# Optimization experiments

Measured on AMD Instinct MI355X. Metric: run time of the kernel, lower is better.

## Reference

```python
import jax, jax.numpy as jnp
from jax import lax
import numpy as np

B, H, W, C = 64, 64, 64, 8          # batch, grid, channel_n (C=8 is structurally required)
PC = 3 * C                           # perceive output channels = 24
FIRE_RATE = 0.5
ALPHA_THR = 0.1

def _conv(x, w, b, padding):
    y = lax.conv_general_dilated(x, w, (1, 1), padding,
                                 dimension_numbers=('NHWC', 'HWIO', 'NHWC'))
    return y + b

def _dwconv(x, k):
    # k: [kh, kw, Cin, mult] (TF depthwise layout) -> grouped conv rhs [kh, kw, 1, Cin*mult]
    kh, kw, cin, m = k.shape
    rhs = k.reshape(kh, kw, 1, cin * m)
    return lax.conv_general_dilated(x, rhs, (1, 1), 'SAME',
                                    dimension_numbers=('NHWC', 'HWIO', 'NHWC'),
                                    feature_group_count=cin)

def _maxpool3(a):
    return lax.reduce_window(a, -jnp.inf, lax.max, (1, 3, 3, 1), (1, 1, 1, 1), 'SAME')

def setup_inputs() -> dict:
    key = jax.random.key(0)
    ks = jax.random.split(key, 12)
    d_flat = H * W * PC                       # 98304
    d_att = 3 * 3 * 24 * 3                    # 648
    s = lambda *sh: 0.02
    return {
        'x': jax.random.normal(ks[0], (B, H, W, C), jnp.float32),
        'update_noise': jax.random.uniform(ks[1], (B, H, W, 1), jnp.float32),
        'W_att': jax.random.normal(ks[2], (d_flat, d_att), jnp.float32) * 0.002,
        'b_att': jax.random.normal(ks[3], (d_att,), jnp.float32) * 0.02,
        'W1': jax.random.normal(ks[4], (3, 3, 3 * PC, 48), jnp.float32) * 0.05,
        'b1': jax.random.normal(ks[5], (48,), jnp.float32) * 0.02,
        'Wt': jax.random.normal(ks[6], (3, 3, 48, 48), jnp.float32) * 0.05,
        'bt': jax.random.normal(ks[7], (48,), jnp.float32) * 0.02,
        'W2': jax.random.normal(ks[8], (1, 1, 48, 128), jnp.float32) * 0.05,
        'b2': jax.random.normal(ks[9], (128,), jnp.float32) * 0.02,
        'W3': jax.random.normal(ks[10], (1, 1, 128, C), jnp.float32) * 0.05,
        'b3': jax.random.normal(ks[11], (C,), jnp.float32) * 0.02,
    }

def reference(x, update_noise, W_att, b_att, W1, b1, Wt, bt, W2, b2, W3, b3):
    # --- fixed perceive stencil (angle = 0) ---
    ident = np.outer(np.float32([0, 1, 0]), np.float32([0, 1, 0]))
    dxk = np.outer(np.float32([1, 0, 1]), np.float32([1, 0, 1])) / 8.0
    dyk = dxk.T
    k = jnp.stack([jnp.asarray(ident), jnp.asarray(dxk), jnp.asarray(dyk)], -1)  # [3,3,3]
    k = jnp.tile(k[:, :, None, :], (1, 1, C, 1))                                 # [3,3,C,3]

    pre_life = _maxpool3(x[:, :, :, 3:4]) > ALPHA_THR

    y = _dwconv(x, k)                                     # [B,H,W,24]
    # global attention: flatten -> dense -> reshape, take sample 0's kernel
    y_sum = (y.reshape(y.shape[0], -1) @ W_att + b_att).reshape(-1, 3, 3, 24, 3)[0]
    y = _dwconv(y, y_sum)                                 # [B,H,W,72]
    y = y * lax.rsqrt(jnp.maximum(jnp.sum(y * y), 1e-12))  # global l2_normalize

    # dmodel: conv3 VALID -> convT3 VALID -> 1x1 relu -> 1x1
    h = _conv(y, W1, b1, 'VALID')                         # [B,62,62,48]
    h = lax.conv_transpose(h, Wt, (1, 1), 'VALID',
                           dimension_numbers=('NHWC', 'HWIO', 'NHWC')) + bt  # [B,64,64,48]
    h = jax.nn.relu(_conv(h, W2, b2, 'SAME'))             # [B,64,64,128]
    dx_out = _conv(h, W3, b3, 'SAME')                     # [B,64,64,C], step_size = 1.0

    update_mask = (update_noise <= FIRE_RATE).astype(x.dtype)
    x2 = x + dx_out * update_mask

    post_life = _maxpool3(x2[:, :, :, 3:4]) > ALPHA_THR
    life = jnp.logical_and(pre_life, post_life).astype(x.dtype)
    return x2 * life
```

## Files before the change

### kernel.cpp

```cpp
#include <hip/hip_runtime.h>

#define NB 64
#define HW 4096

__global__ __launch_bounds__(256) void k_prep(
    const float* __restrict__ W2, float* __restrict__ W2T) {
  for (int i = threadIdx.x; i < 6144; i += 256) {
    int o = i / 48;
    int c = i - o * 48;
    W2T[i] = W2[c * 128 + o];
  }
}

__global__ __launch_bounds__(256) void k_perceive(
    const float* __restrict__ x, float* __restrict__ y_chw,
    float* __restrict__ y0_hwc, float* __restrict__ prelife,
    float* __restrict__ att_zero) {
  int t = threadIdx.x;
  if (blockIdx.x == 0) {
    for (int i = t; i < 649; i += 256) att_zero[i] = 0.f;
  }
  int pix = blockIdx.x * 256 + t;
  int b = pix >> 12;
  int hw = pix & 4095;
  int h = hw >> 6, w = hw & 63;
  const float* xp = x + (size_t)pix * 8;
  bool hm = h > 0, hp = h < 63, wm = w > 0, wp = w < 63;

  float mx = -1e30f;
  #pragma unroll
  for (int di = -1; di <= 1; ++di) {
    if ((unsigned)(h + di) > 63u) continue;
    #pragma unroll
    for (int dj = -1; dj <= 1; ++dj) {
      if ((unsigned)(w + dj) > 63u) continue;
      mx = fmaxf(mx, xp[(di * 64 + dj) * 8 + 3]);
    }
  }
  prelife[pix] = (mx > 0.1f) ? 1.f : 0.f;

  float* yb = y_chw + (size_t)b * 16 * HW + hw;
  bool b0 = (b == 0);
  #pragma unroll
  for (int c = 0; c < 8; ++c) {
    float ctr = xp[c];
    float a00 = (hm && wm) ? xp[(-65) * 8 + c] : 0.f;
    float a02 = (hm && wp) ? xp[(-63) * 8 + c] : 0.f;
    float a20 = (hp && wm) ? xp[(63) * 8 + c] : 0.f;
    float a22 = (hp && wp) ? xp[(65) * 8 + c] : 0.f;
    float d = (a00 + a02 + a20 + a22) * 0.125f;
    yb[(size_t)(c * 2 + 0) * HW] = ctr;
    yb[(size_t)(c * 2 + 1) * HW] = d;
    if (b0) {
      float* y0p = y0_hwc + hw * 24 + c * 3;
      y0p[0] = ctr; y0p[1] = d; y0p[2] = d;
    }
  }
}

__global__ __launch_bounds__(256) void k_att(
    const float* __restrict__ y0, const float* __restrict__ Watt,
    float* __restrict__ att_acc) {
  int t = threadIdx.x;
  int r0 = blockIdx.x * 128;
  float a0 = 0.f, a1 = 0.f, a2 = 0.f;
  for (int r = 0; r < 128; ++r) {
    float yv = y0[r0 + r];
    const float* wr = Watt + (size_t)(r0 + r) * 648;
    a0 = fmaf(yv, wr[t], a0);
    a1 = fmaf(yv, wr[t + 256], a1);
    if (t < 136) a2 = fmaf(yv, wr[t + 512], a2);
  }
  atomicAdd(att_acc + t, a0);
  atomicAdd(att_acc + t + 256, a1);
  if (t < 136) atomicAdd(att_acc + t + 512, a2);
}

__global__ __launch_bounds__(768) void k_fold(
    const float* __restrict__ W1, const float* __restrict__ att_acc,
    const float* __restrict__ b_att, float* __restrict__ K16) {
  __shared__ float ys[648];
  int t = threadIdx.x;
  for (int i = t; i < 648; i += 768) ys[i] = att_acc[i] + b_att[i];
  __syncthreads();
  int r = blockIdx.x;
  int ri = r / 5, rj = r - ri * 5;
  int p = t / 48;
  int o = t - p * 48;
  int c = p >> 1, tt = p & 1;
  float acc = 0.f;
  for (int ki = 0; ki < 3; ++ki) {
    int qi = ri - ki;
    if ((unsigned)qi > 2u) continue;
    for (int kj = 0; kj < 3; ++kj) {
      int qj = rj - kj;
      if ((unsigned)qj > 2u) continue;
      int k9 = ki * 3 + kj, q9 = qi * 3 + qj;
      const float* wb = W1 + (size_t)(k9 * 72 + 9 * c) * 48 + o;
      const float* yb = ys + q9 * 72 + 9 * c;
      if (tt == 0) {
        #pragma unroll
        for (int m = 0; m < 3; ++m) acc = fmaf(wb[(size_t)m * 48], yb[m], acc);
      } else {
        #pragma unroll
        for (int m = 0; m < 3; ++m) {
          acc = fmaf(wb[(size_t)(3 + m) * 48], yb[3 + m], acc);
          acc = fmaf(wb[(size_t)(6 + m) * 48], yb[6 + m], acc);
        }
      }
    }
  }
  K16[(size_t)(r * 16 + p) * 48 + o] = acc;
}

__global__ __launch_bounds__(256) void k_ssq(
    const float* __restrict__ y_chw, const float* __restrict__ att_acc,
    const float* __restrict__ b_att, float* __restrict__ ssq) {
  __shared__ float ys[648];
  __shared__ float s[16 * 324];
  int t = threadIdx.x;
  for (int i = t; i < 648; i += 256) ys[i] = att_acc[i] + b_att[i];

  int blk = blockIdx.x;
  int b = blk >> 4;
  int tile = blk & 15;
  int i0 = (tile >> 2) * 16;
  int j0 = (tile & 3) * 16;
  const float* yb = y_chw + (size_t)b * 16 * HW;

  for (int idx = t; idx < 16 * 324; idx += 256) {
    int c = idx / 324;
    int pos = idx - c * 324;
    int r = pos / 18, col = pos - r * 18;
    int gr = i0 - 1 + r, gc = j0 - 1 + col;
    bool v = ((unsigned)gr < 64u) && ((unsigned)gc < 64u);
    s[idx] = v ? yb[(size_t)c * HW + gr * 64 + gc] : 0.f;
  }
  __syncthreads();

  int ty = t >> 4, tx = t & 15;
  float local = 0.f;
  for (int c = 0; c < 8; ++c) {
    float tapA[9], tapB[9];
    const float* sa = s + (size_t)(2 * c) * 324 + ty * 18 + tx;
    const float* sb = s + (size_t)(2 * c + 1) * 324 + ty * 18 + tx;
    #pragma unroll
    for (int di = 0; di < 3; ++di)
      #pragma unroll
      for (int dj = 0; dj < 3; ++dj) {
        tapA[di * 3 + dj] = sa[di * 18 + dj];
        tapB[di * 3 + dj] = sb[di * 18 + dj];
      }
    #pragma unroll
    for (int m = 0; m < 3; ++m) {
      float z0 = 0.f, z1 = 0.f, z2 = 0.f;
      #pragma unroll
      for (int k9 = 0; k9 < 9; ++k9) {
        z0 = fmaf(tapA[k9], ys[k9 * 72 + 9 * c + m], z0);
        z1 = fmaf(tapB[k9], ys[k9 * 72 + 9 * c + 3 + m], z1);
        z2 = fmaf(tapB[k9], ys[k9 * 72 + 9 * c + 6 + m], z2);
      }
      local += z0 * z0 + z1 * z1 + z2 * z2;
    }
  }
  #pragma unroll
  for (int off = 32; off; off >>= 1) local += __shfl_down(local, off, 64);
  if ((t & 63) == 0) atomicAdd(ssq, local);
}

__global__ __launch_bounds__(256, 4) void k_conv1f(
    const float* __restrict__ y_chw, const float* __restrict__ K16,
    const float* __restrict__ b1, const float* __restrict__ ssqp,
    float* __restrict__ h1) {
  __shared__ float s[16 * 400];
  int t = threadIdx.x;
  int og = __builtin_amdgcn_readfirstlane(t >> 7);
  int sub = t & 127;
  int ty = sub >> 4, tx = sub & 15;
  int blk = blockIdx.x;
  int b = blk >> 4;
  int tile = blk & 15;
  int i0 = (tile >> 2) * 16; if (i0 > 46) i0 = 46;
  int j0 = (tile & 3) * 16;  if (j0 > 46) j0 = 46;

  const float* yb = y_chw + (size_t)b * 16 * HW;
  for (int idx = t; idx < 16 * 400; idx += 256) {
    int c = idx / 400;
    int pos = idx - c * 400;
    int r = pos / 20, col = pos - r * 20;
    int gr = i0 - 1 + r, gc = j0 - 1 + col;
    bool v = ((unsigned)gr < 64u) && ((unsigned)gc < 64u);
    s[idx] = v ? yb[(size_t)c * HW + gr * 64 + gc] : 0.f;
  }
  __syncthreads();

  float acc0[24], acc1[24];
  #pragma unroll
  for (int o = 0; o < 24; ++o) { acc0[o] = 0.f; acc1[o] = 0.f; }

  for (int c = 0; c < 16; ++c) {
    const float* sc = s + (size_t)c * 400 + ty * 20 + tx;
    #pragma unroll
    for (int ri = 0; ri < 5; ++ri) {
      float t0[5], t1[5];
      #pragma unroll
      for (int rj = 0; rj < 5; ++rj) {
        t0[rj] = sc[ri * 20 + rj];
        t1[rj] = sc[(ri + 8) * 20 + rj];
      }
      #pragma unroll
      for (int rj = 0; rj < 5; ++rj) {
        const float* w = K16 + (size_t)((ri * 5 + rj) * 16 + c) * 48 + og * 24;
        float tv0 = t0[rj], tv1 = t1[rj];
        #pragma unroll
        for (int o = 0; o < 24; ++o) {
          acc0[o] = fmaf(tv0, w[o], acc0[o]);
          acc1[o] = fmaf(tv1, w[o], acc1[o]);
        }
      }
    }
  }
  float inv = rsqrtf(fmaxf(ssqp[0], 1e-12f));
  float* hb = h1 + (size_t)b * 48 * 3844 + (size_t)og * 24 * 3844
            + (i0 + ty) * 62 + (j0 + tx);
  #pragma unroll
  for (int o = 0; o < 24; ++o) {
    float bo = b1[og * 24 + o];
    hb[(size_t)o * 3844] = fmaf(acc0[o], inv, bo);
    hb[(size_t)o * 3844 + 8 * 62] = fmaf(acc1[o], inv, bo);
  }
}

__global__ __launch_bounds__(256, 4) void k_convT(
    const float* __restrict__ h1, const float* __restrict__ Wt,
    const float* __restrict__ bt, float* __restrict__ h2) {
  __shared__ float s[24 * 324];
  int t = threadIdx.x;
  int og = __builtin_amdgcn_readfirstlane(t >> 7);
  int sub = t & 127;
  int ty = sub >> 4, tx = sub & 15;
  int blk = blockIdx.x;
  int b = blk >> 4;
  int tile = blk & 15;
  int i0 = (tile >> 2) * 16;
  int j0 = (tile & 3) * 16;

  float acc0[24], acc1[24];
  #pragma unroll
  for (int o = 0; o < 24; ++o) { acc0[o] = 0.f; acc1[o] = 0.f; }
  const float* hb = h1 + (size_t)b * 48 * 3844;

  for (int c0 = 0; c0 < 48; c0 += 24) {
    __syncthreads();
    for (int idx = t; idx < 24 * 324; idx += 256) {
      int c = idx / 324;
      int pos = idx - c * 324;
      int r = pos / 18, col = pos - r * 18;
      int gr = i0 - 2 + r, gc = j0 - 2 + col;
      bool v = ((unsigned)gr < 62u) && ((unsigned)gc < 62u);
      s[idx] = v ? hb[(size_t)(c0 + c) * 3844 + gr * 62 + gc] : 0.f;
    }
    __syncthreads();
    for (int c = 0; c < 24; ++c) {
      const float* sc = s + c * 324 + ty * 18 + tx;
      float tap0[9], tap1[9];
      #pragma unroll
      for (int di = 0; di < 3; ++di)
        #pragma unroll
        for (int dj = 0; dj < 3; ++dj) {
          tap0[di * 3 + dj] = sc[di * 18 + dj];
          tap1[di * 3 + dj] = sc[(di + 8) * 18 + dj];
        }
      #pragma unroll
      for (int k9 = 0; k9 < 9; ++k9) {
        const float* w = Wt + (size_t)(k9 * 48 + c0 + c) * 48 + og * 24;
        float tv0 = tap0[k9], tv1 = tap1[k9];
        #pragma unroll
        for (int o = 0; o < 24; ++o) {
          acc0[o] = fmaf(tv0, w[o], acc0[o]);
          acc1[o] = fmaf(tv1, w[o], acc1[o]);
        }
      }
    }
  }
  float* ob = h2 + (size_t)b * 48 * HW + (size_t)og * 24 * HW
            + (i0 + ty) * 64 + (j0 + tx);
  #pragma unroll
  for (int o = 0; o < 24; ++o) {
    float bo = bt[og * 24 + o];
    ob[(size_t)o * HW] = acc0[o] + bo;
    ob[(size_t)o * HW + 8 * 64] = acc1[o] + bo;
  }
}

__global__ __launch_bounds__(256) void k_head(
    const float* __restrict__ h2, const float* __restrict__ W2T,
    const float* __restrict__ b2, const float* __restrict__ W3,
    const float* __restrict__ b3, const float* __restrict__ x,
    const float* __restrict__ noise, float* __restrict__ x2,
    float* __restrict__ alpha2) {
  int t = threadIdx.x;
  int pix0 = blockIdx.x * 512 + t;
  int pix1 = pix0 + 256;
  int b = pix0 >> 12;
  int hw0 = pix0 & 4095, hw1 = pix1 & 4095;
  float hr0[48], hr1[48];
  const float* hb = h2 + (size_t)b * 48 * HW;
  #pragma unroll
  for (int c = 0; c < 48; ++c) {
    hr0[c] = hb[(size_t)c * HW + hw0];
    hr1[c] = hb[(size_t)c * HW + hw1];
  }
  float dx0[8], dx1[8];
  #pragma unroll
  for (int k = 0; k < 8; ++k) { dx0[k] = b3[k]; dx1[k] = b3[k]; }
  #pragma unroll 2
  for (int o = 0; o < 128; ++o) {
    float v0 = b2[o], v1 = v0;
    const float* w2 = W2T + o * 48;
    #pragma unroll
    for (int c = 0; c < 48; ++c) {
      v0 = fmaf(hr0[c], w2[c], v0);
      v1 = fmaf(hr1[c], w2[c], v1);
    }
    v0 = fmaxf(v0, 0.f);
    v1 = fmaxf(v1, 0.f);
    const float* w3 = W3 + o * 8;
    #pragma unroll
    for (int k = 0; k < 8; ++k) {
      dx0[k] = fmaf(v0, w3[k], dx0[k]);
      dx1[k] = fmaf(v1, w3[k], dx1[k]);
    }
  }
  float m0 = (noise[pix0] <= 0.5f) ? 1.f : 0.f;
  float m1 = (noise[pix1] <= 0.5f) ? 1.f : 0.f;
  const float* xp0 = x + (size_t)pix0 * 8;
  const float* xp1 = x + (size_t)pix1 * 8;
  float* xo0 = x2 + (size_t)pix0 * 8;
  float* xo1 = x2 + (size_t)pix1 * 8;
  float a30 = 0.f, a31 = 0.f;
  #pragma unroll
  for (int k = 0; k < 8; ++k) {
    float v0 = fmaf(dx0[k], m0, xp0[k]);
    float v1 = fmaf(dx1[k], m1, xp1[k]);
    xo0[k] = v0; xo1[k] = v1;
    if (k == 3) { a30 = v0; a31 = v1; }
  }
  alpha2[pix0] = a30;
  alpha2[pix1] = a31;
}

__global__ __launch_bounds__(256) void k_life(
    const float* __restrict__ x2, const float* __restrict__ alpha2,
    const float* __restrict__ prelife, float* __restrict__ out) {
  int pix = blockIdx.x * 256 + threadIdx.x;
  int hw = pix & 4095;
  int h = hw >> 6, w = hw & 63;
  const float* ab = alpha2 + (size_t)(pix - hw);
  float mx = -1e30f;
  #pragma unroll
  for (int di = -1; di <= 1; ++di) {
    if ((unsigned)(h + di) > 63u) continue;
    #pragma unroll
    for (int dj = -1; dj <= 1; ++dj) {
      if ((unsigned)(w + dj) > 63u) continue;
      mx = fmaxf(mx, ab[(h + di) * 64 + (w + dj)]);
    }
  }
  float life = (mx > 0.1f && prelife[pix] > 0.5f) ? 1.f : 0.f;
  const float* xp = x2 + (size_t)pix * 8;
  float* op = out + (size_t)pix * 8;
  #pragma unroll
  for (int k = 0; k < 8; ++k) op[k] = xp[k] * life;
}

extern "C" void kernel_launch(void* const* d_in, const int* in_sizes, int n_in,
                              void* d_out, int out_size, void* d_ws, size_t ws_size,
                              hipStream_t stream) {
  const float* x     = (const float*)d_in[0];
  const float* noise = (const float*)d_in[1];
  const float* Watt  = (const float*)d_in[2];
  const float* b_att = (const float*)d_in[3];
  const float* W1    = (const float*)d_in[4];
  const float* b1    = (const float*)d_in[5];
  const float* Wt    = (const float*)d_in[6];
  const float* bt    = (const float*)d_in[7];
  const float* W2    = (const float*)d_in[8];
  const float* b2    = (const float*)d_in[9];
  const float* W3    = (const float*)d_in[10];
  const float* b3    = (const float*)d_in[11];
  float* out = (float*)d_out;

  float* ws = (float*)d_ws;
  size_t o_y   = 0;
  size_t o_h1  = o_y + 4194304;
  size_t o_h2  = o_h1 + 11808768;
  size_t o_y0  = o_h2 + 12582912;
  size_t o_pre = o_y0 + 98304;
  size_t o_att = o_pre + 262144;
  size_t o_w2t = o_att + 652;
  size_t o_k16 = o_w2t + 6144;
  float* y_chw   = ws + o_y;
  float* h1_chw  = ws + o_h1;
  float* h2_chw  = ws + o_h2;
  float* y0_hwc  = ws + o_y0;
  float* prelife = ws + o_pre;
  float* att_acc = ws + o_att;
  float* ssq     = ws + o_att + 648;
  float* W2T     = ws + o_w2t;
  float* K16     = ws + o_k16;
  float* x2      = ws + o_y;
  float* alpha2  = ws + o_y + 2097152;

  k_prep<<<1, 256, 0, stream>>>(W2, W2T);
  k_perceive<<<1024, 256, 0, stream>>>(x, y_chw, y0_hwc, prelife, att_acc);
  k_att<<<768, 256, 0, stream>>>(y0_hwc, Watt, att_acc);
  k_fold<<<25, 768, 0, stream>>>(W1, att_acc, b_att, K16);
  k_ssq<<<1024, 256, 0, stream>>>(y_chw, att_acc, b_att, ssq);
  k_conv1f<<<1024, 256, 0, stream>>>(y_chw, K16, b1, ssq, h1_chw);
  k_convT<<<1024, 256, 0, stream>>>(h1_chw, Wt, bt, h2_chw);
  k_head<<<512, 256, 0, stream>>>(h2_chw, W2T, b2, W3, b3, x, noise, x2, alpha2);
  k_life<<<1024, 256, 0, stream>>>(x2, alpha2, prelife, out);
}
```

Measured before the change: 888.4 us.

## Fuse convT with 1x1 head, merge prep and fold into neighbor kernels

The transposed conv output tile is staged in shared memory and consumed directly by the 1x1 relu/1x1 head in the same block. This removes the h2 global write and re-read and one launch. The W2 transpose and the K16 fold move into extra blocks of the perceive and ssq kernels, removing two more launches. The price is a larger shared-memory footprint (48x256 floats) and occupancy lowered to 3 blocks/CU. The head now does one pixel per thread instead of two, so weight loads are reused less.

```diff
diff --git a/kernel.cpp b/kernel.cpp
--- a/kernel.cpp
+++ b/kernel.cpp
@@ -2,21 +2,21 @@
 
 #define NB 64
 #define HW 4096
-
-__global__ __launch_bounds__(256) void k_prep(
-    const float* __restrict__ W2, float* __restrict__ W2T) {
-  for (int i = threadIdx.x; i < 6144; i += 256) {
-    int o = i / 48;
-    int c = i - o * 48;
-    W2T[i] = W2[c * 128 + o];
-  }
-}
 
 __global__ __launch_bounds__(256) void k_perceive(
     const float* __restrict__ x, float* __restrict__ y_chw,
     float* __restrict__ y0_hwc, float* __restrict__ prelife,
-    float* __restrict__ att_zero) {
+    float* __restrict__ att_zero, const float* __restrict__ W2,
+    float* __restrict__ W2T) {
   int t = threadIdx.x;
+  if (blockIdx.x == 1024) {
+    for (int i = t; i < 6144; i += 256) {
+      int o = i / 48;
+      int c = i - o * 48;
+      W2T[i] = W2[c * 128 + o];
+    }
+    return;
+  }
   if (blockIdx.x == 0) {
     for (int i = t; i < 649; i += 256) att_zero[i] = 0.f;
   }
@@ -76,49 +76,52 @@
   if (t < 136) atomicAdd(att_acc + t + 512, a2);
 }
 
-__global__ __launch_bounds__(768) void k_fold(
-    const float* __restrict__ W1, const float* __restrict__ att_acc,
-    const float* __restrict__ b_att, float* __restrict__ K16) {
-  __shared__ float ys[648];
-  int t = threadIdx.x;
-  for (int i = t; i < 648; i += 768) ys[i] = att_acc[i] + b_att[i];
-  __syncthreads();
-  int r = blockIdx.x;
-  int ri = r / 5, rj = r - ri * 5;
-  int p = t / 48;
-  int o = t - p * 48;
-  int c = p >> 1, tt = p & 1;
-  float acc = 0.f;
-  for (int ki = 0; ki < 3; ++ki) {
-    int qi = ri - ki;
-    if ((unsigned)qi > 2u) continue;
-    for (int kj = 0; kj < 3; ++kj) {
-      int qj = rj - kj;
-      if ((unsigned)qj > 2u) continue;
-      int k9 = ki * 3 + kj, q9 = qi * 3 + qj;
-      const float* wb = W1 + (size_t)(k9 * 72 + 9 * c) * 48 + o;
-      const float* yb = ys + q9 * 72 + 9 * c;
-      if (tt == 0) {
-        #pragma unroll
-        for (int m = 0; m < 3; ++m) acc = fmaf(wb[(size_t)m * 48], yb[m], acc);
-      } else {
-        #pragma unroll
-        for (int m = 0; m < 3; ++m) {
-          acc = fmaf(wb[(size_t)(3 + m) * 48], yb[3 + m], acc);
-          acc = fmaf(wb[(size_t)(6 + m) * 48], yb[6 + m], acc);
-        }
-      }
-    }
-  }
-  K16[(size_t)(r * 16 + p) * 48 + o] = acc;
-}
-
-__global__ __launch_bounds__(256) void k_ssq(
+__global__ __launch_bounds__(256) void k_ssqfold(
     const float* __restrict__ y_chw, const float* __restrict__ att_acc,
-    const float* __restrict__ b_att, float* __restrict__ ssq) {
+    const float* __restrict__ b_att, float* __restrict__ ssq,
+    const float* __restrict__ W1, float* __restrict__ K16) {
   __shared__ float ys[648];
   __shared__ float s[16 * 324];
   int t = threadIdx.x;
+
+  if (blockIdx.x >= 1024) {
+    for (int i = t; i < 648; i += 256) ys[i] = att_acc[i] + b_att[i];
+    __syncthreads();
+    int r = blockIdx.x - 1024;
+    int ri = r / 5, rj = r - ri * 5;
+    #pragma unroll
+    for (int k = 0; k < 3; ++k) {
+      int idx = t + 256 * k;
+      int p = idx / 48;
+      int o = idx - p * 48;
+      int c = p >> 1, tt = p & 1;
+      float acc = 0.f;
+      for (int ki = 0; ki < 3; ++ki) {
+        int qi = ri - ki;
+        if ((unsigned)qi > 2u) continue;
+        for (int kj = 0; kj < 3; ++kj) {
+          int qj = rj - kj;
+          if ((unsigned)qj > 2u) continue;
+          int k9 = ki * 3 + kj, q9 = qi * 3 + qj;
+          const float* wb = W1 + (size_t)(k9 * 72 + 9 * c) * 48 + o;
+          const float* yb = ys + q9 * 72 + 9 * c;
+          if (tt == 0) {
+            #pragma unroll
+            for (int m = 0; m < 3; ++m) acc = fmaf(wb[(size_t)m * 48], yb[m], acc);
+          } else {
+            #pragma unroll
+            for (int m = 0; m < 3; ++m) {
+              acc = fmaf(wb[(size_t)(3 + m) * 48], yb[3 + m], acc);
+              acc = fmaf(wb[(size_t)(6 + m) * 48], yb[6 + m], acc);
+            }
+          }
+        }
+      }
+      K16[(size_t)(r * 16 + p) * 48 + o] = acc;
+    }
+    return;
+  }
+
   for (int i = t; i < 648; i += 256) ys[i] = att_acc[i] + b_att[i];
 
   int blk = blockIdx.x;
@@ -231,10 +234,14 @@
   }
 }
 
-__global__ __launch_bounds__(256, 4) void k_convT(
+__global__ __launch_bounds__(256, 3) void k_convTh(
     const float* __restrict__ h1, const float* __restrict__ Wt,
-    const float* __restrict__ bt, float* __restrict__ h2) {
-  __shared__ float s[24 * 324];
+    const float* __restrict__ bt, const float* __restrict__ W2T,
+    const float* __restrict__ b2, const float* __restrict__ W3,
+    const float* __restrict__ b3, const float* __restrict__ x,
+    const float* __restrict__ noise, float* __restrict__ x2,
+    float* __restrict__ alpha2) {
+  __shared__ float s[48 * 256];
   int t = threadIdx.x;
   int og = __builtin_amdgcn_readfirstlane(t >> 7);
   int sub = t & 127;
@@ -283,71 +290,47 @@
       }
     }
   }
-  float* ob = h2 + (size_t)b * 48 * HW + (size_t)og * 24 * HW
-            + (i0 + ty) * 64 + (j0 + tx);
+
+  __syncthreads();
   #pragma unroll
   for (int o = 0; o < 24; ++o) {
     float bo = bt[og * 24 + o];
-    ob[(size_t)o * HW] = acc0[o] + bo;
-    ob[(size_t)o * HW + 8 * 64] = acc1[o] + bo;
-  }
-}
-
-__global__ __launch_bounds__(256) void k_head(
-    const float* __restrict__ h2, const float* __restrict__ W2T,
-    const float* __restrict__ b2, const float* __restrict__ W3,
-    const float* __restrict__ b3, const float* __restrict__ x,
-    const float* __restrict__ noise, float* __restrict__ x2,
-    float* __restrict__ alpha2) {
-  int t = threadIdx.x;
-  int pix0 = blockIdx.x * 512 + t;
-  int pix1 = pix0 + 256;
-  int b = pix0 >> 12;
-  int hw0 = pix0 & 4095, hw1 = pix1 & 4095;
-  float hr0[48], hr1[48];
-  const float* hb = h2 + (size_t)b * 48 * HW;
-  #pragma unroll
-  for (int c = 0; c < 48; ++c) {
-    hr0[c] = hb[(size_t)c * HW + hw0];
-    hr1[c] = hb[(size_t)c * HW + hw1];
-  }
-  float dx0[8], dx1[8];
-  #pragma unroll
-  for (int k = 0; k < 8; ++k) { dx0[k] = b3[k]; dx1[k] = b3[k]; }
+    s[(og * 24 + o) * 256 + ty * 16 + tx] = acc0[o] + bo;
+    s[(og * 24 + o) * 256 + (ty + 8) * 16 + tx] = acc1[o] + bo;
+  }
+  __syncthreads();
+
+  int pty = t >> 4, ptx = t & 15;
+  int pix = b * 4096 + (i0 + pty) * 64 + (j0 + ptx);
+  float hr[48];
+  #pragma unroll
+  for (int c = 0; c < 48; ++c) hr[c] = s[c * 256 + t];
+
+  float dx[8];
+  #pragma unroll
+  for (int k = 0; k < 8; ++k) dx[k] = b3[k];
   #pragma unroll 2
   for (int o = 0; o < 128; ++o) {
-    float v0 = b2[o], v1 = v0;
+    float v = b2[o];
     const float* w2 = W2T + o * 48;
     #pragma unroll
-    for (int c = 0; c < 48; ++c) {
-      v0 = fmaf(hr0[c], w2[c], v0);
-      v1 = fmaf(hr1[c], w2[c], v1);
-    }
-    v0 = fmaxf(v0, 0.f);
-    v1 = fmaxf(v1, 0.f);
+    for (int c = 0; c < 48; ++c) v = fmaf(hr[c], w2[c], v);
+    v = fmaxf(v, 0.f);
     const float* w3 = W3 + o * 8;
     #pragma unroll
-    for (int k = 0; k < 8; ++k) {
-      dx0[k] = fmaf(v0, w3[k], dx0[k]);
-      dx1[k] = fmaf(v1, w3[k], dx1[k]);
-    }
-  }
-  float m0 = (noise[pix0] <= 0.5f) ? 1.f : 0.f;
-  float m1 = (noise[pix1] <= 0.5f) ? 1.f : 0.f;
-  const float* xp0 = x + (size_t)pix0 * 8;
-  const float* xp1 = x + (size_t)pix1 * 8;
-  float* xo0 = x2 + (size_t)pix0 * 8;
-  float* xo1 = x2 + (size_t)pix1 * 8;
-  float a30 = 0.f, a31 = 0.f;
+    for (int k = 0; k < 8; ++k) dx[k] = fmaf(v, w3[k], dx[k]);
+  }
+  float m = (noise[pix] <= 0.5f) ? 1.f : 0.f;
+  const float* xp = x + (size_t)pix * 8;
+  float* xo = x2 + (size_t)pix * 8;
+  float a3 = 0.f;
   #pragma unroll
   for (int k = 0; k < 8; ++k) {
-    float v0 = fmaf(dx0[k], m0, xp0[k]);
-    float v1 = fmaf(dx1[k], m1, xp1[k]);
-    xo0[k] = v0; xo1[k] = v1;
-    if (k == 3) { a30 = v0; a31 = v1; }
-  }
-  alpha2[pix0] = a30;
-  alpha2[pix1] = a31;
+    float v = fmaf(dx[k], m, xp[k]);
+    xo[k] = v;
+    if (k == 3) a3 = v;
+  }
+  alpha2[pix] = a3;
 }
 
 __global__ __launch_bounds__(256) void k_life(
@@ -394,15 +377,13 @@
   float* ws = (float*)d_ws;
   size_t o_y   = 0;
   size_t o_h1  = o_y + 4194304;
-  size_t o_h2  = o_h1 + 11808768;
-  size_t o_y0  = o_h2 + 12582912;
+  size_t o_y0  = o_h1 + 11808768;
   size_t o_pre = o_y0 + 98304;
   size_t o_att = o_pre + 262144;
   size_t o_w2t = o_att + 652;
   size_t o_k16 = o_w2t + 6144;
   float* y_chw   = ws + o_y;
   float* h1_chw  = ws + o_h1;
-  float* h2_chw  = ws + o_h2;
   float* y0_hwc  = ws + o_y0;
   float* prelife = ws + o_pre;
   float* att_acc = ws + o_att;
@@ -412,13 +393,10 @@
   float* x2      = ws + o_y;
   float* alpha2  = ws + o_y + 2097152;
 
-  k_prep<<<1, 256, 0, stream>>>(W2, W2T);
-  k_perceive<<<1024, 256, 0, stream>>>(x, y_chw, y0_hwc, prelife, att_acc);
+  k_perceive<<<1025, 256, 0, stream>>>(x, y_chw, y0_hwc, prelife, att_acc, W2, W2T);
   k_att<<<768, 256, 0, stream>>>(y0_hwc, Watt, att_acc);
-  k_fold<<<25, 768, 0, stream>>>(W1, att_acc, b_att, K16);
-  k_ssq<<<1024, 256, 0, stream>>>(y_chw, att_acc, b_att, ssq);
+  k_ssqfold<<<1049, 256, 0, stream>>>(y_chw, att_acc, b_att, ssq, W1, K16);
   k_conv1f<<<1024, 256, 0, stream>>>(y_chw, K16, b1, ssq, h1_chw);
-  k_convT<<<1024, 256, 0, stream>>>(h1_chw, Wt, bt, h2_chw);
-  k_head<<<512, 256, 0, stream>>>(h2_chw, W2T, b2, W3, b3, x, noise, x2, alpha2);
+  k_convTh<<<1024, 256, 0, stream>>>(h1_chw, Wt, bt, W2T, b2, W3, b3, x, noise, x2, alpha2);
   k_life<<<1024, 256, 0, stream>>>(x2, alpha2, prelife, out);
 }
```

Result: slower. 947.9 us (+6.7%).
